# Performance work log

Measured on AMD Instinct MI355X. Metric: run time of the kernel, lower is better.

## Reference

```python
import jax, jax.numpy as jnp
import numpy as np

FP8_MAX = 448.0  # float8_e4m3fn max representable
BLOCK = 64       # Hadamard block size (non-H20 branch)


def _hadamard(size):
    m2 = np.array([[1.0, 1.0], [1.0, -1.0]], dtype=np.float32)
    h = m2
    for _ in range(int(np.log2(size)) - 1):
        h = np.kron(h, m2)
    return jnp.asarray(h / np.sqrt(size), dtype=jnp.float32)


def _block_rotate(x, H):
    # x: (M, K), K % BLOCK == 0; block-diagonal Hadamard rotation along last dim
    M, K = x.shape
    b = H.shape[0]
    return (x.reshape(M, K // b, b) @ H).reshape(M, K)


def _quant_fp8(x):
    # per-row absmax scaling into float8_e4m3fn
    s = jnp.max(jnp.abs(x), axis=-1, keepdims=True) / FP8_MAX
    s = jnp.maximum(s, 1e-12)
    q = (x / s).astype(jnp.float8_e4m3fn)
    return q, s[:, 0]


def hadamard_quant(a, H):
    # emulates triton_hadamard_quant's non-transposed outputs (fwd only needs these)
    return _quant_fp8(_block_rotate(a, H))


def _scaled_mm(aq, a_scale, bq, b_scale, out_dtype=jnp.float32):
    # torch._scaled_mm(aq, bq.t(), scale_a=a_scale[:,None], scale_b=b_scale[None,:])
    out = jnp.matmul(aq.astype(jnp.float32), bq.astype(jnp.float32).T)
    return (out * a_scale[:, None] * b_scale[None, :]).astype(out_dtype)


def setup_inputs() -> dict:
    key = jax.random.key(0)
    k1, k2 = jax.random.split(key)
    B, S, K, N = 4, 8192, 1024, 1024
    x = jax.random.normal(k1, (B, S, K), dtype=jnp.float32)
    w = 0.02 * jax.random.normal(k2, (N, K), dtype=jnp.float32)  # reset_parameters std=0.02
    b = jnp.zeros((N,), dtype=jnp.float32)
    H = _hadamard(BLOCK)
    return {"input": x, "weight": w, "bias": b, "hadamard_matrix": H}


def reference(input, weight, bias, hadamard_matrix):
    x2d = input.reshape(-1, input.shape[-1])            # (M, K)
    x_q, x_s = hadamard_quant(x2d, hadamard_matrix)     # fp8 (M, K), scales (M,)
    w_q, w_s = hadamard_quant(weight, hadamard_matrix)  # fp8 (N, K), scales (N,)
    out = _scaled_mm(x_q, x_s, w_q, w_s) + bias         # (M, N)
    return out.reshape(*input.shape[:-1], -1)
```

## Files before the change

kernel.cpp:

```cpp
#include <hip/hip_runtime.h>
#include <cstdint>

typedef __attribute__((ext_vector_type(4))) float f32x4;


#define KDIM 1024
#define NBLK 16

__global__ __launch_bounds__(256) void hq_quant_kernel(
    const float* __restrict__ x, const float* __restrict__ w,
    uint8_t* __restrict__ xq, uint8_t* __restrict__ wq,
    float* __restrict__ xs, float* __restrict__ wsc, int mrows, int nrows) {
  __shared__ float lds[4][1280];
  const int lane = threadIdx.x & 63;
  const int wave = threadIdx.x >> 6;
  const int gwave = (blockIdx.x * blockDim.x + threadIdx.x) >> 6;
  const int wstride = (gridDim.x * blockDim.x) >> 6;
  const int total = mrows + nrows;
  float* L = lds[wave];

  for (int r = gwave; r < total; r += wstride) {
    const float* src = (r < mrows) ? (x + (size_t)r * KDIM)
                                   : (w + (size_t)(r - mrows) * KDIM);
    uint8_t* dst = (r < mrows) ? (xq + (size_t)r * KDIM)
                               : (wq + (size_t)(r - mrows) * KDIM);
    float* sdst = (r < mrows) ? (xs + r) : (wsc + (r - mrows));

    float v[NBLK];
#pragma unroll
    for (int b = 0; b < NBLK; ++b) v[b] = src[b * 64 + lane];

#pragma unroll
    for (int s = 1; s < 64; s <<= 1) {
#pragma unroll
      for (int b = 0; b < NBLK; ++b) {
        float o = __shfl_xor(v[b], s, 64);
        v[b] = (lane & s) ? (o - v[b]) : (v[b] + o);
      }
    }

    float amax = 0.f;
#pragma unroll
    for (int b = 0; b < NBLK; ++b) {
      v[b] *= 0.125f;
      amax = fmaxf(amax, fabsf(v[b]));
    }
#pragma unroll
    for (int s = 32; s >= 1; s >>= 1) amax = fmaxf(amax, __shfl_xor(amax, s, 64));

    float scale = fmaxf(amax / 448.0f, 1e-12f);

#pragma unroll
    for (int b = 0; b < NBLK; ++b) {
      int c = b * 64 + lane;
      L[c + 4 * (c >> 4)] = v[b];
    }
    __builtin_amdgcn_wave_barrier();

    uint32_t pk[4];
#pragma unroll
    for (int g = 0; g < 4; ++g) {
      f32x4 f = *reinterpret_cast<const f32x4*>(&L[20 * lane + 4 * g]);
      float q0 = f[0] / scale, q1 = f[1] / scale;
      float q2 = f[2] / scale, q3 = f[3] / scale;
      int p = __builtin_amdgcn_cvt_pk_fp8_f32(q0, q1, 0, false);
      p = __builtin_amdgcn_cvt_pk_fp8_f32(q2, q3, p, true);
      pk[g] = (uint32_t)p;
    }
    *reinterpret_cast<uint4*>(dst + lane * 16) =
        make_uint4(pk[0], pk[1], pk[2], pk[3]);
    if (lane == 0) *sdst = scale;
    __builtin_amdgcn_wave_barrier();
  }
}


__device__ __forceinline__ void gload16(const uint8_t* g, uint8_t* l) {
  __builtin_amdgcn_global_load_lds(
      (const __attribute__((address_space(1))) void*)g,
      (__attribute__((address_space(3))) void*)l, 16, 0, 0);
}

__global__ __launch_bounds__(256) void hq_gemm_kernel(
    const uint8_t* __restrict__ Aq, const uint8_t* __restrict__ Bq,
    const float* __restrict__ As, const float* __restrict__ Bs,
    const float* __restrict__ bias, float* __restrict__ C, int M, int N,
    int Kd) {
  constexpr int BM = 128, BN = 128, BK = 64;
  __shared__ uint8_t sA[BM * BK];
  __shared__ uint8_t sB[BN * BK];
  const int tid = threadIdx.x;
  const int lane = tid & 63;
  const int wave = tid >> 6;
  const int ntn = N / BN;
  const int tileM = (int)(blockIdx.x / ntn) * BM;
  const int tileN = (int)(blockIdx.x % ntn) * BN;
  const int wm = (wave >> 1) * 64;
  const int wn = (wave & 1) * 64;
  const int fr = lane & 15;
  const int fq = lane >> 4;

  f32x4 acc[4][4] = {};

  const int so = tid * 16;
  const int srow = so >> 6;
  const int scol = so & 63;
  const uint8_t* gA0 = Aq + (size_t)(tileM + srow) * Kd + scol;
  const uint8_t* gA1 = Aq + (size_t)(tileM + srow + 64) * Kd + scol;
  const uint8_t* gB0 = Bq + (size_t)(tileN + srow) * Kd + scol;
  const uint8_t* gB1 = Bq + (size_t)(tileN + srow + 64) * Kd + scol;

  for (int k0 = 0; k0 < Kd; k0 += BK) {
    __syncthreads();
    gload16(gA0 + k0, sA + so);
    gload16(gA1 + k0, sA + so + 4096);
    gload16(gB0 + k0, sB + so);
    gload16(gB1 + k0, sB + so + 4096);
    __syncthreads();

    long a[2][4], b[2][4];
#pragma unroll
    for (int ks = 0; ks < 2; ++ks) {
#pragma unroll
      for (int mf = 0; mf < 4; ++mf)
        a[ks][mf] =
            *(const long*)(sA + (wm + mf * 16 + fr) * 64 + ks * 32 + fq * 8);
#pragma unroll
      for (int nf = 0; nf < 4; ++nf)
        b[ks][nf] =
            *(const long*)(sB + (wn + nf * 16 + fr) * 64 + ks * 32 + fq * 8);
    }
#pragma unroll
    for (int ks = 0; ks < 2; ++ks)
#pragma unroll
      for (int mf = 0; mf < 4; ++mf)
#pragma unroll
        for (int nf = 0; nf < 4; ++nf)
          acc[mf][nf] = __builtin_amdgcn_mfma_f32_16x16x32_fp8_fp8(
              a[ks][mf], b[ks][nf], acc[mf][nf], 0, 0, 0);
  }

  float bscale[4], bbias[4];
#pragma unroll
  for (int nf = 0; nf < 4; ++nf) {
    int col = tileN + wn + nf * 16 + fr;
    bscale[nf] = Bs[col];
    bbias[nf] = bias[col];
  }
#pragma unroll
  for (int mf = 0; mf < 4; ++mf) {
    int r0 = tileM + wm + mf * 16 + fq * 4;
#pragma unroll
    for (int i = 0; i < 4; ++i) {
      float as = As[r0 + i];
      float* crow = C + (size_t)(r0 + i) * N;
#pragma unroll
      for (int nf = 0; nf < 4; ++nf) {
        int col = tileN + wn + nf * 16 + fr;
        crow[col] = acc[mf][nf][i] * as * bscale[nf] + bbias[nf];
      }
    }
  }
}


extern "C" void kernel_launch(void* const* d_in, const int* in_sizes, int n_in,
                              void* d_out, int out_size, void* d_ws,
                              size_t ws_size, hipStream_t stream) {
  const float* x = (const float*)d_in[0];
  const float* w = (const float*)d_in[1];
  const float* bias = (const float*)d_in[2];

  const int N = in_sizes[2];
  const int Kd = in_sizes[1] / N;
  const int M = in_sizes[0] / Kd;
  float* out = (float*)d_out;

  uint8_t* xq = (uint8_t*)d_ws;
  uint8_t* wq = xq + (size_t)M * Kd;
  float* xs = (float*)(wq + (size_t)N * Kd);
  float* wsc = xs + M;

  hq_quant_kernel<<<2048, 256, 0, stream>>>(x, w, xq, wq, xs, wsc, M, N);

  dim3 grid((M / 128) * (N / 128));
  hq_gemm_kernel<<<grid, 256, 0, stream>>>(xq, wq, xs, wsc, bias, out, M, N,
                                           Kd);
}
```

Measured before the change: 359.1 us.

## Double-buffer GEMM LDS with swizzle and simplify Hadamard quant via float4

The GEMM now uses two LDS buffers so global-to-LDS loads for the next K tile overlap MFMA work on the current one. It also XOR-swizzles the LDS layout to reduce bank conflicts and remaps workgroup IDs for better cache locality. The quant kernel loads float4s, performs the first two butterfly stages in registers and the rest with 16-lane shuffles, then writes fp8 bytes directly without an LDS transpose. This doubles GEMM LDS usage, which may reduce occupancy.

```diff
diff --git a/kernel.cpp b/kernel.cpp
--- a/kernel.cpp
+++ b/kernel.cpp
@@ -5,19 +5,15 @@
 
 
 #define KDIM 1024
-#define NBLK 16
 
 __global__ __launch_bounds__(256) void hq_quant_kernel(
     const float* __restrict__ x, const float* __restrict__ w,
     uint8_t* __restrict__ xq, uint8_t* __restrict__ wq,
     float* __restrict__ xs, float* __restrict__ wsc, int mrows, int nrows) {
-  __shared__ float lds[4][1280];
   const int lane = threadIdx.x & 63;
-  const int wave = threadIdx.x >> 6;
   const int gwave = (blockIdx.x * blockDim.x + threadIdx.x) >> 6;
   const int wstride = (gridDim.x * blockDim.x) >> 6;
   const int total = mrows + nrows;
-  float* L = lds[wave];
 
   for (int r = gwave; r < total; r += wstride) {
     const float* src = (r < mrows) ? (x + (size_t)r * KDIM)
@@ -26,51 +22,54 @@
                                : (wq + (size_t)(r - mrows) * KDIM);
     float* sdst = (r < mrows) ? (xs + r) : (wsc + (r - mrows));
 
-    float v[NBLK];
-#pragma unroll
-    for (int b = 0; b < NBLK; ++b) v[b] = src[b * 64 + lane];
-
-#pragma unroll
-    for (int s = 1; s < 64; s <<= 1) {
-#pragma unroll
-      for (int b = 0; b < NBLK; ++b) {
-        float o = __shfl_xor(v[b], s, 64);
-        v[b] = (lane & s) ? (o - v[b]) : (v[b] + o);
+    f32x4 v[4];
+    const f32x4* s4 = reinterpret_cast<const f32x4*>(src);
+#pragma unroll
+    for (int g = 0; g < 4; ++g) v[g] = s4[g * 64 + lane];
+
+#pragma unroll
+    for (int g = 0; g < 4; ++g) {
+      float a0 = v[g][0], a1 = v[g][1], a2 = v[g][2], a3 = v[g][3];
+      float b0 = a0 + a1, b1 = a0 - a1, b2 = a2 + a3, b3 = a2 - a3;
+      v[g][0] = b0 + b2;
+      v[g][1] = b1 + b3;
+      v[g][2] = b0 - b2;
+      v[g][3] = b1 - b3;
+    }
+#pragma unroll
+    for (int sl = 1; sl <= 8; sl <<= 1) {
+      const bool hi = (lane & sl) != 0;
+#pragma unroll
+      for (int g = 0; g < 4; ++g)
+#pragma unroll
+        for (int t = 0; t < 4; ++t) {
+          float o = __shfl_xor(v[g][t], sl, 64);
+          v[g][t] = hi ? (o - v[g][t]) : (v[g][t] + o);
+        }
+    }
+
+    float amax = 0.f;
+#pragma unroll
+    for (int g = 0; g < 4; ++g)
+#pragma unroll
+      for (int t = 0; t < 4; ++t) {
+        v[g][t] *= 0.125f;
+        amax = fmaxf(amax, fabsf(v[g][t]));
       }
-    }
-
-    float amax = 0.f;
-#pragma unroll
-    for (int b = 0; b < NBLK; ++b) {
-      v[b] *= 0.125f;
-      amax = fmaxf(amax, fabsf(v[b]));
-    }
-#pragma unroll
-    for (int s = 32; s >= 1; s >>= 1) amax = fmaxf(amax, __shfl_xor(amax, s, 64));
-
-    float scale = fmaxf(amax / 448.0f, 1e-12f);
-
-#pragma unroll
-    for (int b = 0; b < NBLK; ++b) {
-      int c = b * 64 + lane;
-      L[c + 4 * (c >> 4)] = v[b];
-    }
-    __builtin_amdgcn_wave_barrier();
-
-    uint32_t pk[4];
+#pragma unroll
+    for (int s = 1; s < 64; s <<= 1) amax = fmaxf(amax, __shfl_xor(amax, s, 64));
+
+    const float scale = fmaxf(amax / 448.0f, 1e-12f);
+
 #pragma unroll
     for (int g = 0; g < 4; ++g) {
-      f32x4 f = *reinterpret_cast<const f32x4*>(&L[20 * lane + 4 * g]);
-      float q0 = f[0] / scale, q1 = f[1] / scale;
-      float q2 = f[2] / scale, q3 = f[3] / scale;
-      int p = __builtin_amdgcn_cvt_pk_fp8_f32(q0, q1, 0, false);
-      p = __builtin_amdgcn_cvt_pk_fp8_f32(q2, q3, p, true);
-      pk[g] = (uint32_t)p;
-    }
-    *reinterpret_cast<uint4*>(dst + lane * 16) =
-        make_uint4(pk[0], pk[1], pk[2], pk[3]);
+      int p = __builtin_amdgcn_cvt_pk_fp8_f32(v[g][0] / scale, v[g][1] / scale,
+                                              0, false);
+      p = __builtin_amdgcn_cvt_pk_fp8_f32(v[g][2] / scale, v[g][3] / scale, p,
+                                          true);
+      reinterpret_cast<uint32_t*>(dst)[g * 64 + lane] = (uint32_t)p;
+    }
     if (lane == 0) *sdst = scale;
-    __builtin_amdgcn_wave_barrier();
   }
 }
 
@@ -87,14 +86,19 @@
     const float* __restrict__ bias, float* __restrict__ C, int M, int N,
     int Kd) {
   constexpr int BM = 128, BN = 128, BK = 64;
-  __shared__ uint8_t sA[BM * BK];
-  __shared__ uint8_t sB[BN * BK];
+  __shared__ uint8_t sA0[BM * BK], sB0[BN * BK];
+  __shared__ uint8_t sA1[BM * BK], sB1[BN * BK];
   const int tid = threadIdx.x;
   const int lane = tid & 63;
   const int wave = tid >> 6;
   const int ntn = N / BN;
-  const int tileM = (int)(blockIdx.x / ntn) * BM;
-  const int tileN = (int)(blockIdx.x % ntn) * BN;
+
+  const int nwg = gridDim.x;
+  const int bid = blockIdx.x;
+  const int wg = (bid & 7) * (nwg >> 3) + (bid >> 3);
+
+  const int tileM = (wg / ntn) * BM;
+  const int tileN = (wg % ntn) * BN;
   const int wm = (wave >> 1) * 64;
   const int wn = (wave & 1) * 64;
   const int fr = lane & 15;
@@ -105,30 +109,30 @@
   const int so = tid * 16;
   const int srow = so >> 6;
   const int scol = so & 63;
-  const uint8_t* gA0 = Aq + (size_t)(tileM + srow) * Kd + scol;
-  const uint8_t* gA1 = Aq + (size_t)(tileM + srow + 64) * Kd + scol;
-  const uint8_t* gB0 = Bq + (size_t)(tileN + srow) * Kd + scol;
-  const uint8_t* gB1 = Bq + (size_t)(tileN + srow + 64) * Kd + scol;
-
-  for (int k0 = 0; k0 < Kd; k0 += BK) {
-    __syncthreads();
-    gload16(gA0 + k0, sA + so);
-    gload16(gA1 + k0, sA + so + 4096);
-    gload16(gB0 + k0, sB + so);
-    gload16(gB1 + k0, sB + so + 4096);
-    __syncthreads();
-
+  const int scsw = scol ^ ((srow & 3) << 4);
+  const uint8_t* gA0 = Aq + (size_t)(tileM + srow) * Kd + scsw;
+  const uint8_t* gA1 = Aq + (size_t)(tileM + srow + 64) * Kd + scsw;
+  const uint8_t* gB0 = Bq + (size_t)(tileN + srow) * Kd + scsw;
+  const uint8_t* gB1 = Bq + (size_t)(tileN + srow + 64) * Kd + scsw;
+
+  auto stage = [&](uint8_t* dA, uint8_t* dB, int k0) {
+    gload16(gA0 + k0, dA + so);
+    gload16(gA1 + k0, dA + so + 4096);
+    gload16(gB0 + k0, dB + so);
+    gload16(gB1 + k0, dB + so + 4096);
+  };
+
+  auto compute = [&](const uint8_t* dA, const uint8_t* dB) {
     long a[2][4], b[2][4];
 #pragma unroll
     for (int ks = 0; ks < 2; ++ks) {
+      const int csw = (ks * 32 + fq * 8) ^ ((fr & 3) << 4);
 #pragma unroll
       for (int mf = 0; mf < 4; ++mf)
-        a[ks][mf] =
-            *(const long*)(sA + (wm + mf * 16 + fr) * 64 + ks * 32 + fq * 8);
+        a[ks][mf] = *(const long*)(dA + (wm + mf * 16 + fr) * 64 + csw);
 #pragma unroll
       for (int nf = 0; nf < 4; ++nf)
-        b[ks][nf] =
-            *(const long*)(sB + (wn + nf * 16 + fr) * 64 + ks * 32 + fq * 8);
+        b[ks][nf] = *(const long*)(dB + (wn + nf * 16 + fr) * 64 + csw);
     }
 #pragma unroll
     for (int ks = 0; ks < 2; ++ks)
@@ -138,7 +142,24 @@
         for (int nf = 0; nf < 4; ++nf)
           acc[mf][nf] = __builtin_amdgcn_mfma_f32_16x16x32_fp8_fp8(
               a[ks][mf], b[ks][nf], acc[mf][nf], 0, 0, 0);
-  }
+  };
+
+  stage(sA0, sB0, 0);
+  __syncthreads();
+
+  int k0 = 0;
+  for (; k0 + 2 * BK < Kd; k0 += 2 * BK) {
+    stage(sA1, sB1, k0 + BK);
+    compute(sA0, sB0);
+    __syncthreads();
+    stage(sA0, sB0, k0 + 2 * BK);
+    compute(sA1, sB1);
+    __syncthreads();
+  }
+  stage(sA1, sB1, k0 + BK);
+  compute(sA0, sB0);
+  __syncthreads();
+  compute(sA1, sB1);
 
   float bscale[4], bbias[4];
 #pragma unroll
```

Result: faster. 295.4 us (-17.7%).
